# Kernel optimization log

Measured on AMD Instinct MI355X. Metric: run time of the kernel, lower is better.

## Reference

```python
import jax, jax.numpy as jnp
import numpy as np

NUM_UNIQUE = 256      # unique initial states after unique_bitstrings_with_counts
NUM_SAMPLES = 4096    # expectation_samples (shots per unique circuit)
NUM_QUBITS = 64
BATCH_SIZE = 1024


def setup_inputs() -> dict:
    key = jax.random.key(0)
    k1, k2, k3, k4 = jax.random.split(key, 4)
    # Bitstring samples drawn from each unique transformed circuit (stands in
    # for tfq.layers.Sample output, already densified like .to_tensor()).
    samples = jax.random.randint(k1, (NUM_UNIQUE, NUM_SAMPLES, NUM_QUBITS), 0, 2, dtype=jnp.int32)
    # expand_unique_results gather indices: batch entry -> unique circuit id
    idx = jax.random.randint(k2, (BATCH_SIZE,), 0, NUM_UNIQUE, dtype=jnp.int32)
    # Ising/KOBE energy parameters (observable.energy thetas)
    bias = jax.random.normal(k3, (NUM_QUBITS,), dtype=jnp.float32)
    kernel = jax.random.normal(k4, (NUM_QUBITS, NUM_QUBITS), dtype=jnp.float32) * 0.1
    return {"samples": samples, "idx": idx, "bias": bias, "kernel": kernel}


def reference(samples, idx, bias, kernel):
    # spins s = 1 - 2*b  for bitstrings b in {0,1}
    spins = 1.0 - 2.0 * samples.astype(jnp.float32)          # [c, s, q]
    # observable.energy(x): linear + quadratic Ising energy per bitstring
    lin = jnp.einsum("csq,q->cs", spins, bias)                # [c, s]
    quad = jnp.einsum("csq,qr,csr->cs", spins, kernel, spins)  # [c, s]
    energies = lin + quad
    # tf.map_fn(reduce_mean(energy)) over unique circuits -> [c]
    unique_expectations = jnp.mean(energies, axis=1)
    # expand_unique_results: gather back to full batch, expand_dims(..., 1)
    return unique_expectations[idx][:, None]                  # [batch_size, 1]
```

## Files before the change

### kernel.cpp

```cpp
#include <hip/hip_runtime.h>
#include <stdint.h>

#define NUM_UNIQUE   256
#define NUM_SAMPLES  4096
#define NUM_QUBITS   64
#define BATCH_SIZE   1024
#define THREADS      1024
#define WAVES        (THREADS / 64)
#define CHUNKS       (NUM_SAMPLES / 64)
#define CHUNKS_PER_WAVE (CHUNKS / WAVES)

typedef int v4i __attribute__((ext_vector_type(4)));

__global__ __launch_bounds__(THREADS)
void energy_kernel(const int* __restrict__ samples,
                   const float* __restrict__ bias,
                   const float* __restrict__ Kmat,
                   float* __restrict__ uniq)
{
    __shared__ float Klds[NUM_QUBITS * 65];
    __shared__ unsigned long long words[WAVES][64];
    __shared__ float wsum[WAVES];

    const int tid  = threadIdx.x;
    const int wave = tid >> 6;
    const int lane = tid & 63;
    const int c    = blockIdx.x;

    for (int t = tid; t < NUM_QUBITS * NUM_QUBITS; t += THREADS)
        Klds[(t >> 6) * 65 + (t & 63)] = Kmat[t];
    __syncthreads();

    const float* Krow = &Klds[lane * 65];
    float rowsum = 0.0f;
    #pragma unroll
    for (int r = 0; r < 64; ++r) rowsum += Krow[r];

    float pcacc = 0.0f;
    int   cnt   = 0;

    const int loadrot  = (3 * wave + 5 * c) & 15;
    const int chunkrot = (13 * c) & 63;

    for (int ci = 0; ci < CHUNKS_PER_WAVE; ++ci) {
        const int chunk = ((wave * CHUNKS_PER_WAVE + ci) + chunkrot) & 63;
        const v4i* cp = (const v4i*)(samples +
            ((size_t)c * NUM_SAMPLES + (size_t)chunk * 64) * NUM_QUBITS);

        unsigned int m0 = 0, m1 = 0, m2 = 0, m3 = 0;
        #pragma unroll
        for (int i = 0; i < 16; ++i) {
            const int j = (i + loadrot) & 15;
            v4i v = __builtin_nontemporal_load(cp + j * 64 + lane);
            m0 = (m0 << 1) | (unsigned int)(v.x & 1);
            m1 = (m1 << 1) | (unsigned int)(v.y & 1);
            m2 = (m2 << 1) | (unsigned int)(v.z & 1);
            m3 = (m3 << 1) | (unsigned int)(v.w & 1);
        }
        unsigned long long W = (unsigned long long)m0
                             | ((unsigned long long)m1 << 16)
                             | ((unsigned long long)m2 << 32)
                             | ((unsigned long long)m3 << 48);

        unsigned long long B = 0ull;
        #pragma unroll
        for (int p = 0; p < 4; ++p) {
            unsigned long long src = __shfl(W, 16 * p + (lane >> 2));
            B |= ((src >> (16 * (lane & 3))) & 0xFFFFull) << (16 * p);
        }

        cnt += (int)__popcll(B);
        words[wave][lane] = B;

        const unsigned long long* wp = words[wave];
        #pragma unroll
        for (int r = 0; r < 64; ++r) {
            unsigned long long br = wp[r];
            int pc = (int)__popcll(B ^ br);
            pcacc = fmaf(Krow[r], (float)pc, pcacc);
        }
    }

    float contrib = 64.0f * (float)CHUNKS_PER_WAVE * rowsum - 2.0f * pcacc
                  + bias[lane] * (float)(CHUNKS_PER_WAVE * 64 - 2 * cnt);

    #pragma unroll
    for (int off = 32; off > 0; off >>= 1)
        contrib += __shfl_down(contrib, off);

    if (lane == 0) wsum[wave] = contrib;
    __syncthreads();
    if (tid == 0) {
        float s = 0.0f;
        #pragma unroll
        for (int i = 0; i < WAVES; ++i) s += wsum[i];
        uniq[c] = s * (1.0f / NUM_SAMPLES);
    }
}

__global__ void gather_kernel(const float* __restrict__ uniq,
                              const int* __restrict__ idx,
                              float* __restrict__ out)
{
    int b = blockIdx.x * blockDim.x + threadIdx.x;
    if (b < BATCH_SIZE) out[b] = uniq[idx[b]];
}

extern "C" void kernel_launch(void* const* d_in, const int* in_sizes, int n_in,
                              void* d_out, int out_size, void* d_ws, size_t ws_size,
                              hipStream_t stream)
{
    const int*   samples = (const int*)d_in[0];
    const int*   idx     = (const int*)d_in[1];
    const float* bias    = (const float*)d_in[2];
    const float* Kmat    = (const float*)d_in[3];
    float* out  = (float*)d_out;
    float* uniq = (float*)d_ws;

    energy_kernel<<<NUM_UNIQUE, THREADS, 0, stream>>>(samples, bias, Kmat, uniq);
    gather_kernel<<<(BATCH_SIZE + 255) / 256, 256, 0, stream>>>(uniq, idx, out);
}
```

Baseline: 349.2 us.

## Split each circuit across four blocks, symmetrize kernel, and prefetch sample chunks

Each unique circuit is now processed by four 256-thread blocks instead of one 1024-thread block, and the partial sums are combined in the gather kernel. The pairwise popcount loop uses a symmetrized kernel (K+K^T) over 32 cyclic offsets, which halves the XOR/popcount/FMA work per chunk; a duplicated word buffer handles the wraparound. The next chunk's sample loads are issued into registers before the current chunk is processed, overlapping memory latency with compute. The costs are higher register pressure from the 16-element prefetch buffer, extra LDS for the symmetric table, and the removal of the earlier address rotation intended to spread memory traffic.

```diff
diff --git a/kernel.cpp b/kernel.cpp
--- a/kernel.cpp
+++ b/kernel.cpp
@@ -5,79 +5,110 @@
 #define NUM_SAMPLES  4096
 #define NUM_QUBITS   64
 #define BATCH_SIZE   1024
-#define THREADS      1024
-#define WAVES        (THREADS / 64)
-#define CHUNKS       (NUM_SAMPLES / 64)
-#define CHUNKS_PER_WAVE (CHUNKS / WAVES)
+
+#define THREADS      256
+#define WAVES        4
+#define BLOCKS_PER_C 4
+#define GRID         (NUM_UNIQUE * BLOCKS_PER_C)
+#define CHUNKS_PER_WAVE 4
+#define CHUNK_V4     1024
 
 typedef int v4i __attribute__((ext_vector_type(4)));
+typedef unsigned long long u64;
 
-__global__ __launch_bounds__(THREADS)
+__global__ __launch_bounds__(THREADS, 4)
 void energy_kernel(const int* __restrict__ samples,
                    const float* __restrict__ bias,
                    const float* __restrict__ Kmat,
-                   float* __restrict__ uniq)
+                   float* __restrict__ part)
 {
     __shared__ float Klds[NUM_QUBITS * 65];
-    __shared__ unsigned long long words[WAVES][64];
+    __shared__ float KS[NUM_QUBITS * 33];
+    __shared__ u64   words[WAVES][128];
     __shared__ float wsum[WAVES];
 
     const int tid  = threadIdx.x;
     const int wave = tid >> 6;
     const int lane = tid & 63;
-    const int c    = blockIdx.x;
+    const int blk  = blockIdx.x;
+    const int c    = blk >> 2;
+    const int sub  = blk & 3;
+
+    const int chunk0 = sub * 16 + wave * CHUNKS_PER_WAVE;
+    const v4i* cp = (const v4i*)samples
+                  + (size_t)c * (NUM_SAMPLES * NUM_QUBITS / 4)
+                  + (size_t)chunk0 * CHUNK_V4;
+
+    v4i L[16];
+    #pragma unroll
+    for (int i = 0; i < 16; ++i)
+        L[i] = __builtin_nontemporal_load(cp + i * 64 + lane);
 
     for (int t = tid; t < NUM_QUBITS * NUM_QUBITS; t += THREADS)
         Klds[(t >> 6) * 65 + (t & 63)] = Kmat[t];
     __syncthreads();
 
-    const float* Krow = &Klds[lane * 65];
+    for (int t = tid; t < 64 * 32; t += THREADS) {
+        int q = t >> 5, d = (t & 31) + 1, r = (q + d) & 63;
+        float v = Klds[q * 65 + r] + Klds[r * 65 + q];
+        KS[q * 33 + d] = (d == 32) ? 0.5f * v : v;
+    }
+
     float rowsum = 0.0f;
-    #pragma unroll
-    for (int r = 0; r < 64; ++r) rowsum += Krow[r];
+    {
+        const float* Krow = &Klds[lane * 65];
+        #pragma unroll
+        for (int r = 0; r < 64; ++r) rowsum += Krow[r];
+    }
+    __syncthreads();
+
+    const float* ks = &KS[lane * 33];
+    u64* wrow       = &words[wave][0];
+    const u64* wp   = &words[wave][lane];
 
     float pcacc = 0.0f;
     int   cnt   = 0;
 
-    const int loadrot  = (3 * wave + 5 * c) & 15;
-    const int chunkrot = (13 * c) & 63;
-
+    #pragma unroll
     for (int ci = 0; ci < CHUNKS_PER_WAVE; ++ci) {
-        const int chunk = ((wave * CHUNKS_PER_WAVE + ci) + chunkrot) & 63;
-        const v4i* cp = (const v4i*)(samples +
-            ((size_t)c * NUM_SAMPLES + (size_t)chunk * 64) * NUM_QUBITS);
-
         unsigned int m0 = 0, m1 = 0, m2 = 0, m3 = 0;
         #pragma unroll
         for (int i = 0; i < 16; ++i) {
-            const int j = (i + loadrot) & 15;
-            v4i v = __builtin_nontemporal_load(cp + j * 64 + lane);
+            v4i v = L[i];
             m0 = (m0 << 1) | (unsigned int)(v.x & 1);
             m1 = (m1 << 1) | (unsigned int)(v.y & 1);
             m2 = (m2 << 1) | (unsigned int)(v.z & 1);
             m3 = (m3 << 1) | (unsigned int)(v.w & 1);
         }
-        unsigned long long W = (unsigned long long)m0
-                             | ((unsigned long long)m1 << 16)
-                             | ((unsigned long long)m2 << 32)
-                             | ((unsigned long long)m3 << 48);
 
-        unsigned long long B = 0ull;
+        if (ci + 1 < CHUNKS_PER_WAVE) {
+            const v4i* np = cp + (size_t)(ci + 1) * CHUNK_V4;
+            #pragma unroll
+            for (int i = 0; i < 16; ++i)
+                L[i] = __builtin_nontemporal_load(np + i * 64 + lane);
+        }
+
+        u64 W = (u64)m0 | ((u64)m1 << 16) | ((u64)m2 << 32) | ((u64)m3 << 48);
+
+        u64 B = 0ull;
         #pragma unroll
         for (int p = 0; p < 4; ++p) {
-            unsigned long long src = __shfl(W, 16 * p + (lane >> 2));
+            u64 src = __shfl(W, 16 * p + (lane >> 2));
             B |= ((src >> (16 * (lane & 3))) & 0xFFFFull) << (16 * p);
         }
 
         cnt += (int)__popcll(B);
-        words[wave][lane] = B;
 
-        const unsigned long long* wp = words[wave];
+        asm volatile("" ::: "memory");
+        wrow[lane]      = B;
+        wrow[lane + 64] = B;
+        asm volatile("" ::: "memory");
+
         #pragma unroll
-        for (int r = 0; r < 64; ++r) {
-            unsigned long long br = wp[r];
+        for (int d = 1; d <= 32; ++d) {
+            u64 br = wp[d];
             int pc = (int)__popcll(B ^ br);
-            pcacc = fmaf(Krow[r], (float)pc, pcacc);
+            pcacc = fmaf(ks[d], (float)pc, pcacc);
         }
     }
 
@@ -90,20 +121,20 @@
 
     if (lane == 0) wsum[wave] = contrib;
     __syncthreads();
-    if (tid == 0) {
-        float s = 0.0f;
-        #pragma unroll
-        for (int i = 0; i < WAVES; ++i) s += wsum[i];
-        uniq[c] = s * (1.0f / NUM_SAMPLES);
-    }
+    if (tid == 0)
+        part[blk] = wsum[0] + wsum[1] + wsum[2] + wsum[3];
 }
 
-__global__ void gather_kernel(const float* __restrict__ uniq,
+__global__ void gather_kernel(const float* __restrict__ part,
                               const int* __restrict__ idx,
                               float* __restrict__ out)
 {
     int b = blockIdx.x * blockDim.x + threadIdx.x;
-    if (b < BATCH_SIZE) out[b] = uniq[idx[b]];
+    if (b < BATCH_SIZE) {
+        int u = idx[b] << 2;
+        out[b] = (part[u] + part[u + 1] + part[u + 2] + part[u + 3])
+               * (1.0f / NUM_SAMPLES);
+    }
 }
 
 extern "C" void kernel_launch(void* const* d_in, const int* in_sizes, int n_in,
@@ -115,8 +146,8 @@
     const float* bias    = (const float*)d_in[2];
     const float* Kmat    = (const float*)d_in[3];
     float* out  = (float*)d_out;
-    float* uniq = (float*)d_ws;
+    float* part = (float*)d_ws;
 
-    energy_kernel<<<NUM_UNIQUE, THREADS, 0, stream>>>(samples, bias, Kmat, uniq);
-    gather_kernel<<<(BATCH_SIZE + 255) / 256, 256, 0, stream>>>(uniq, idx, out);
+    energy_kernel<<<GRID, THREADS, 0, stream>>>(samples, bias, Kmat, part);
+    gather_kernel<<<(BATCH_SIZE + THREADS - 1) / THREADS, THREADS, 0, stream>>>(part, idx, out);
 }
```

After: 373.9 us. +7.1%, slower.

## Exploit symmetric pair sum to halve popcount loop and fuse gather into energy kernel

Applied to the files above, without the earlier changes.

Builds a folded symmetric kernel table KS (K[q][r]+K[r][q] over cyclic offsets 1..32, halving the d=32 term) so each lane does 32 popcount-FMA steps per chunk instead of 64. Each bit word is written twice into LDS so lanes can read it by cyclic offset. The separate gather kernel is removed: each block writes its expectation to every batch slot whose idx matches its circuit, which saves one launch. The kernel is likely bound on loading the 256 MB of samples, so halving the compute loop may not help much.

```diff
diff --git a/kernel.cpp b/kernel.cpp
--- a/kernel.cpp
+++ b/kernel.cpp
@@ -11,16 +11,20 @@
 #define CHUNKS_PER_WAVE (CHUNKS / WAVES)
 
 typedef int v4i __attribute__((ext_vector_type(4)));
+typedef unsigned long long u64;
 
 __global__ __launch_bounds__(THREADS)
 void energy_kernel(const int* __restrict__ samples,
+                   const int* __restrict__ idx,
                    const float* __restrict__ bias,
                    const float* __restrict__ Kmat,
-                   float* __restrict__ uniq)
+                   float* __restrict__ out)
 {
     __shared__ float Klds[NUM_QUBITS * 65];
-    __shared__ unsigned long long words[WAVES][64];
+    __shared__ float KS[NUM_QUBITS * 33];
+    __shared__ u64   words[WAVES][128];
     __shared__ float wsum[WAVES];
+    __shared__ float uval;
 
     const int tid  = threadIdx.x;
     const int wave = tid >> 6;
@@ -31,10 +35,23 @@
         Klds[(t >> 6) * 65 + (t & 63)] = Kmat[t];
     __syncthreads();
 
-    const float* Krow = &Klds[lane * 65];
+    for (int t = tid; t < 64 * 32; t += THREADS) {
+        int q = t >> 5, d = (t & 31) + 1, r = (q + d) & 63;
+        float v = Klds[q * 65 + r] + Klds[r * 65 + q];
+        KS[q * 33 + d] = (d == 32) ? 0.5f * v : v;
+    }
+
     float rowsum = 0.0f;
-    #pragma unroll
-    for (int r = 0; r < 64; ++r) rowsum += Krow[r];
+    {
+        const float* Krow = &Klds[lane * 65];
+        #pragma unroll
+        for (int r = 0; r < 64; ++r) rowsum += Krow[r];
+    }
+    __syncthreads();
+
+    const float* ks = &KS[lane * 33];
+    u64* wrow       = &words[wave][0];
+    const u64* wp   = &words[wave][lane];
 
     float pcacc = 0.0f;
     int   cnt   = 0;
@@ -57,27 +74,27 @@
             m2 = (m2 << 1) | (unsigned int)(v.z & 1);
             m3 = (m3 << 1) | (unsigned int)(v.w & 1);
         }
-        unsigned long long W = (unsigned long long)m0
-                             | ((unsigned long long)m1 << 16)
-                             | ((unsigned long long)m2 << 32)
-                             | ((unsigned long long)m3 << 48);
+        u64 W = (u64)m0 | ((u64)m1 << 16) | ((u64)m2 << 32) | ((u64)m3 << 48);
 
-        unsigned long long B = 0ull;
+        u64 B = 0ull;
         #pragma unroll
         for (int p = 0; p < 4; ++p) {
-            unsigned long long src = __shfl(W, 16 * p + (lane >> 2));
+            u64 src = __shfl(W, 16 * p + (lane >> 2));
             B |= ((src >> (16 * (lane & 3))) & 0xFFFFull) << (16 * p);
         }
 
         cnt += (int)__popcll(B);
-        words[wave][lane] = B;
 
-        const unsigned long long* wp = words[wave];
+        asm volatile("" ::: "memory");
+        wrow[lane]      = B;
+        wrow[lane + 64] = B;
+        asm volatile("" ::: "memory");
+
         #pragma unroll
-        for (int r = 0; r < 64; ++r) {
-            unsigned long long br = wp[r];
+        for (int d = 1; d <= 32; ++d) {
+            u64 br = wp[d];
             int pc = (int)__popcll(B ^ br);
-            pcacc = fmaf(Krow[r], (float)pc, pcacc);
+            pcacc = fmaf(ks[d], (float)pc, pcacc);
         }
     }
 
@@ -94,16 +111,12 @@
         float s = 0.0f;
         #pragma unroll
         for (int i = 0; i < WAVES; ++i) s += wsum[i];
-        uniq[c] = s * (1.0f / NUM_SAMPLES);
+        uval = s * (1.0f / NUM_SAMPLES);
     }
-}
+    __syncthreads();
 
-__global__ void gather_kernel(const float* __restrict__ uniq,
-                              const int* __restrict__ idx,
-                              float* __restrict__ out)
-{
-    int b = blockIdx.x * blockDim.x + threadIdx.x;
-    if (b < BATCH_SIZE) out[b] = uniq[idx[b]];
+    const float u = uval;
+    if (idx[tid] == c) out[tid] = u;
 }
 
 extern "C" void kernel_launch(void* const* d_in, const int* in_sizes, int n_in,
@@ -114,9 +127,7 @@
     const int*   idx     = (const int*)d_in[1];
     const float* bias    = (const float*)d_in[2];
     const float* Kmat    = (const float*)d_in[3];
-    float* out  = (float*)d_out;
-    float* uniq = (float*)d_ws;
+    float* out = (float*)d_out;
 
-    energy_kernel<<<NUM_UNIQUE, THREADS, 0, stream>>>(samples, bias, Kmat, uniq);
-    gather_kernel<<<(BATCH_SIZE + 255) / 256, 256, 0, stream>>>(uniq, idx, out);
+    energy_kernel<<<NUM_UNIQUE, THREADS, 0, stream>>>(samples, idx, bias, Kmat, out);
 }
```

Result: faster. 340.0 us, median of 2 (-2.6%).
